# Performance work log

Measured on AMD Instinct MI355X. Metric: run time of the kernel, lower is better.

The kernel has to match this reference:

```python
import jax, jax.numpy as jnp
import numpy as np
import math

N, E, C, NB, NEL, NG = 8192, 131072, 64, 8, 4, 16
R_MAX, AVG_NEI, P_CUT, NL, SH = 5.0, 16.0, 6, 2, 16


def _sph(u):
    # real spherical harmonics l=0..3, component normalization (sum_m Y_lm^2 = 2l+1 on unit sphere)
    x, y, z = u[:, 0], u[:, 1], u[:, 2]
    s3, s15, s5 = math.sqrt(3.0), math.sqrt(15.0), math.sqrt(5.0)
    s105, s7 = math.sqrt(105.0), math.sqrt(7.0)
    c35, c21 = math.sqrt(35.0 / 8.0), math.sqrt(21.0 / 8.0)
    Y = [jnp.ones_like(x),
         s3 * x, s3 * y, s3 * z,
         s15 * x * y, s15 * y * z, 0.5 * s5 * (3 * z * z - 1), s15 * x * z, 0.5 * s15 * (x * x - y * y),
         c35 * y * (3 * x * x - y * y), s105 * x * y * z, c21 * y * (5 * z * z - 1),
         0.5 * s7 * (5 * z ** 3 - 3 * z), c21 * x * (5 * z * z - 1),
         0.5 * s105 * z * (x * x - y * y), c35 * x * (x * x - 3 * y * y)]
    return jnp.stack(Y, axis=-1)  # [E,16]


def _bessel(r):
    k = jnp.arange(1, NB + 1, dtype=r.dtype)
    return math.sqrt(2.0 / R_MAX) * jnp.sin(k * jnp.pi * r[:, None] / R_MAX) / r[:, None]


def _poly_cutoff(r):
    p = float(P_CUT)
    x = r / R_MAX
    f = (1.0 - 0.5 * (p + 1) * (p + 2) * x ** p + p * (p + 2) * x ** (p + 1)
         - 0.5 * p * (p + 1) * x ** (p + 2))
    return f * (x < 1.0)


def setup_inputs() -> dict:
    key = jax.random.key(0)
    ks = jax.random.split(key, 16)
    sc = lambda fan: 1.0 / math.sqrt(fan)
    return {
        "pos": 2.0 * jax.random.normal(ks[0], (N, 3), jnp.float32),
        "atom_types": jax.random.randint(ks[1], (N,), 0, NEL),
        "edge_index": jax.random.randint(ks[2], (2, E), 0, N),
        "batch": jnp.sort(jax.random.randint(ks[3], (N,), 0, NG)),
        "W_embed": jax.random.normal(ks[4], (NEL, C), jnp.float32),
        "W_r1": sc(NB) * jax.random.normal(ks[5], (NL, NB, 64), jnp.float32),
        "W_r2": sc(64) * jax.random.normal(ks[6], (NL, 64, 64), jnp.float32),
        "W_r3": sc(64) * jax.random.normal(ks[7], (NL, 64, C), jnp.float32),
        "W_sc": sc(C) * jax.random.normal(ks[8], (NL, NEL, C, C), jnp.float32),
        "w_prod": 0.5 * jax.random.normal(ks[9], (NL, NEL, 4), jnp.float32),
        "w_ro0": sc(C) * jax.random.normal(ks[10], (C,), jnp.float32),
        "W_ro1a": sc(C) * jax.random.normal(ks[11], (C, 16), jnp.float32),
        "w_ro1b": sc(16) * jax.random.normal(ks[12], (16,), jnp.float32),
    }


def reference(pos, atom_types, edge_index, batch, W_embed, W_r1, W_r2, W_r3,
              W_sc, w_prod, w_ro0, W_ro1a, w_ro1b):
    src, dst = edge_index[0], edge_index[1]
    vec = pos[dst] - pos[src]                      # [E,3]
    r = jnp.sqrt(jnp.sum(vec * vec, -1) + 1e-12)   # [E]
    Y = _sph(vec / r[:, None])                     # [E,SH]
    edge_feats = _bessel(r) * _poly_cutoff(r)[:, None]  # [E,NB]
    h = W_embed[atom_types]                        # one-hot @ W == lookup, [N,C]
    energies = [jnp.zeros((NG,), pos.dtype)]       # pair_repulsion disabled
    for i in range(NL):
        Rw = jax.nn.silu(edge_feats @ W_r1[i])
        Rw = jax.nn.silu(Rw @ W_r2[i])
        Rw = Rw @ W_r3[i]                          # radial MLP weights [E,C]
        # gather-TP-scatter: message [E,C,SH] -> node A [N,C,SH]
        m = (Rw * h[src])[:, :, None] * Y[:, None, :]
        A = jax.ops.segment_sum(m.reshape(E, C * SH), dst,
                                num_segments=N).reshape(N, C, SH) / AVG_NEI
        sc_feat = jnp.einsum('nc,ncd->nd', h, W_sc[i][atom_types])  # element-dep skip
        inv = jnp.stack([A[:, :, 0],
                         jnp.sum(A[:, :, 1:4] ** 2, -1),
                         jnp.sum(A[:, :, 4:9] ** 2, -1),
                         jnp.sum(A[:, :, 9:16] ** 2, -1)], axis=-1)  # [N,C,4]
        h = jnp.einsum('ncj,nj->nc', inv, w_prod[i][atom_types]) + sc_feat
        if i < NL - 1:
            e_node = h @ w_ro0                     # linear readout
        else:
            e_node = jax.nn.silu(h @ W_ro1a) @ w_ro1b  # gated MLP readout
        energies.append(jax.ops.segment_sum(e_node, batch, num_segments=NG))
    contributions = jnp.stack(energies, -1)        # [NG, NL+1]
    return jnp.sum(contributions, -1)              # total energy per graph
```

## Files before the change

kernel.cpp:

```cpp
#include <hip/hip_runtime.h>
#include <hip/hip_bf16.h>
#include <math.h>

#define N_NODES 8192
#define N_EDGES 131072
#define NGRP 16
#define NLAY 2
#define NELM 4
#define SLOT_STRIDE 64
#define N_SLOTS (N_NODES*SLOT_STRIDE)
constexpr float INV_AVG = 1.0f / 16.0f;
constexpr float PI_F = 3.14159265358979323846f;

#define CV_EMB   0
#define CV_SC    256
#define CV_PROD  33024
#define CV_RO0   33056
#define CV_RO1A  33120
#define CV_RO1B  34144
#define CV_SC0T  34160
#define CVT_WORK 34160
#define CVT_N    34416

#define SWZ_PER_L 10240
#define SWZ_N     20480

#define B_GEOM 512
#define B_CVT  134
#define B_SWZ  80
#define SETUP_GRID (B_GEOM + B_CVT + B_SWZ + 1)

typedef __hip_bfloat16 bf16;
typedef __attribute__((ext_vector_type(8))) short bf16x8;
typedef __attribute__((ext_vector_type(4))) float f32x4;

__device__ __forceinline__ float silu_f(float x){ return x / (1.0f + __expf(-x)); }
__device__ __forceinline__ float bfbits2f(unsigned short u){
  return __uint_as_float(((unsigned)u) << 16);
}
__device__ __forceinline__ void unpack2(unsigned u, float& lo, float& hi){
  lo = __uint_as_float(u << 16);
  hi = __uint_as_float(u & 0xffff0000u);
}
__device__ __forceinline__ short f2bs(float v){
  union { bf16 b; short s; } u; u.b = __float2bfloat16(v); return u.s;
}
__device__ __forceinline__ float ldf(const void* p, int i, int flag){
  if (flag) return bfbits2f(((const unsigned short*)p)[i]);
  return ((const float*)p)[i];
}
__device__ __forceinline__ int detect_fl(const void* pos){
  int lane = threadIdx.x & 63;
  const unsigned short* u = (const unsigned short*)pos;
  float va = bfbits2f(u[2*lane]), vb = bfbits2f(u[2*lane+1]);
  bool bad = !(fabsf(va) <= 1000.0f) || !(fabsf(vb) <= 1000.0f);
  return (__ballot(bad) == 0ull) ? 1 : 0;
}
__device__ __forceinline__ void WSYNC(){ __builtin_amdgcn_wave_barrier(); }

__device__ __forceinline__ void gl_lds4(const void* g, void* l){
  __builtin_amdgcn_global_load_lds(
      (const __attribute__((address_space(1))) unsigned*)g,
      (__attribute__((address_space(3))) unsigned*)l, 4, 0, 0);
}

__global__ void k_setup(const void* __restrict__ pos, const int* __restrict__ types,
                        const int* __restrict__ ei,
                        const void* __restrict__ Wemb, const void* __restrict__ Wsc,
                        const void* __restrict__ wprod, const void* __restrict__ wro0,
                        const void* __restrict__ Wro1a, const void* __restrict__ wro1b,
                        const void* __restrict__ Wr1, const void* __restrict__ Wr2,
                        const void* __restrict__ Wr3,
                        int* __restrict__ cursor, uint4* __restrict__ meta,
                        unsigned short* __restrict__ Yb,
                        float* __restrict__ cv, short* __restrict__ swz){
  int b = blockIdx.x, tix = threadIdx.x;
  int fl = detect_fl(pos);
  if (b < B_GEOM){
    int e = b*256 + tix;
    int s = ei[e], d = ei[N_EDGES + e];
    int slot = (d << 6) + atomicAdd(&cursor[d], 1);
    float vx = ldf(pos, d*3+0, fl) - ldf(pos, s*3+0, fl);
    float vy = ldf(pos, d*3+1, fl) - ldf(pos, s*3+1, fl);
    float vz = ldf(pos, d*3+2, fl) - ldf(pos, s*3+2, fl);
    float r = sqrtf(vx*vx + vy*vy + vz*vz + 1e-12f);
    float ir = 1.0f / r;
    float x = vx*ir, y = vy*ir, z = vz*ir;
    const float s3 = 1.7320508075688772f, s15 = 3.872983346207417f, s5 = 2.23606797749979f;
    const float s105 = 10.246950765959598f, s7 = 2.6457513110645907f;
    const float c35 = 2.091650066335189f, c21 = 1.6201851746019651f;
    float x2 = x*x, y2 = y*y, z2 = z*z;
    float ys[16] = {
      1.0f, s3*x, s3*y, s3*z,
      s15*x*y, s15*y*z, 0.5f*s5*(3.0f*z2-1.0f), s15*x*z,
      0.5f*s15*(x2-y2), c35*y*(3.0f*x2-y2), s105*x*y*z, c21*y*(5.0f*z2-1.0f),
      0.5f*s7*(5.0f*z2*z-3.0f*z), c21*x*(5.0f*z2-1.0f), 0.5f*s105*z*(x2-y2),
      c35*x*(x2-3.0f*y2) };
    union { bf16 bb[16]; uint4 u[2]; } pk;
#pragma unroll
    for (int k = 0; k < 16; k++) pk.bb[k] = __float2bfloat16(ys[k]);
    uint4* yp = (uint4*)(Yb + (size_t)e*16);
    yp[0] = pk.u[0];
    yp[1] = pk.u[1];
    meta[slot] = make_uint4((unsigned)s | ((unsigned)types[s] << 16),
                            (unsigned)e, __float_as_uint(r), 0u);
    return;
  }
  if (b < B_GEOM + B_CVT){
    int i = (b - B_GEOM)*256 + tix;
    if (i < 256)  { cv[CV_EMB + i] = ldf(Wemb, i, fl); return; }
    if (i < 33024){ int j=i-256;   cv[CV_SC  + j] = ldf(Wsc,  j, fl); return; }
    if (i < 33056){ int j=i-33024; cv[CV_PROD+ j] = ldf(wprod,j, fl); return; }
    if (i < 33120){ int j=i-33056; cv[CV_RO0 + j] = ldf(wro0, j, fl); return; }
    if (i < 34144){ int j=i-33120; cv[CV_RO1A+ j] = ldf(Wro1a,j, fl); return; }
    if (i < CVT_WORK){ int j=i-34144; cv[CV_RO1B+ j] = ldf(wro1b,j, fl); return; }
    return;
  }
  if (b < B_GEOM + B_CVT + B_SWZ){
    int i = (b - B_GEOM - B_CVT)*256 + tix;
    int l = i / SWZ_PER_L, w = i % SWZ_PER_L;
    float v;
    if (w < 2048){
      int t = w >> 9, q = (w >> 7) & 3, n = (w >> 3) & 15, j = w & 7;
      int k = q*8 + j;
      v = (k < 8) ? ldf(Wr1, l*512 + k*64 + t*16 + n, fl) : 0.0f;
    } else if (w < 6144){
      int w2 = w - 2048;
      int nt = w2 >> 10, kt = (w2 >> 9) & 1, q = (w2 >> 7) & 3, n = (w2 >> 3) & 15, j = w2 & 7;
      int k = kt*32 + q*8 + j;
      v = ldf(Wr2, l*4096 + k*64 + nt*16 + n, fl);
    } else {
      int w3 = w - 6144;
      int nt = w3 >> 10, kt = (w3 >> 9) & 1, q = (w3 >> 7) & 3, n = (w3 >> 3) & 15, j = w3 & 7;
      int k = kt*32 + q*8 + j;
      v = ldf(Wr3, l*4096 + k*64 + nt*16 + n, fl);
    }
    swz[i] = f2bs(v);
    return;
  }
  {
    int ty = tix >> 6, d = tix & 63;
    float s = 0.0f;
#pragma unroll 8
    for (int c = 0; c < 64; c++)
      s += ldf(Wemb, ty*64 + c, fl) * ldf(Wsc, ty*4096 + c*64 + d, fl);
    cv[CV_SC0T + tix] = s;
  }
}

#define ROWS 72
template<int LAYER_KIND>
__global__ void __launch_bounds__(64) k_gu(const short* __restrict__ sw,
        const uint4* __restrict__ meta,
        const float* __restrict__ h_old,
        float* __restrict__ h_new, const unsigned short* __restrict__ Yb,
        const int* __restrict__ cursor, const int* __restrict__ types,
        const float* __restrict__ Wsc, const float* __restrict__ wprod,
        const float* __restrict__ wemb, const float* __restrict__ sc0t,
        const float* __restrict__ wro0,
        const float* __restrict__ Wro1a, const float* __restrict__ wro1b,
        const int* __restrict__ batch, float* __restrict__ ene2){
  __shared__ __align__(16) short A_[16*ROWS];
  __shared__ __align__(16) float hS[LAYER_KIND ? 16 : 1][64];
  __shared__ __align__(16) unsigned short yS[16][16];
  __shared__ float hn_l[64];
  int lane = threadIdx.x;
  int q = lane >> 4, nn = lane & 15;
  int n = blockIdx.x;
  int beg = n << 6;
  short* A = A_;

  const bf16x8* S1 = (const bf16x8*)(sw);
  const bf16x8* S2 = (const bf16x8*)(sw + 2048);
  const bf16x8* S3 = (const bf16x8*)(sw + 6144);

  float e0=0.f, e1=0.f, e2=0.f, e3=0.f;
  if (LAYER_KIND == 0){
    e0 = wemb[lane]; e1 = wemb[64+lane]; e2 = wemb[128+lane]; e3 = wemb[192+lane];
  }

  int dcnt = cursor[n];
  uint4 mC = meta[beg + nn];
  int end = beg + dcnt;

  float acc[16];
#pragma unroll
  for (int s = 0; s < 16; s++) acc[s] = 0.0f;

  int cb = beg;
  do {
    int cnt = min(16, end - cb);
    WSYNC();
    int ev = (int)mC.y;
    {
      int er0 = __shfl(ev, (lane >> 3)) & (N_EDGES - 1);
      gl_lds4((const char*)Yb + (size_t)er0*32 + (lane & 7)*4, &yS[0][0]);
      int er1 = __shfl(ev, 8 + (lane >> 3)) & (N_EDGES - 1);
      gl_lds4((const char*)Yb + (size_t)er1*32 + (lane & 7)*4, &yS[8][0]);
    }
    int tv = (int)((mC.x >> 16) & 3u);
    if (LAYER_KIND == 1){
      int sv = (int)(mC.x & 0xFFFFu);
      for (int i = 0; i < cnt; i++){
        int src = __builtin_amdgcn_readlane(sv, i) & (N_NODES - 1);
        gl_lds4(h_old + (size_t)src*64 + lane, &hS[i][0]);
      }
    }
    float rv = __uint_as_float(mC.z);
    uint4 mN = meta[min(cb + 16 + nn, N_SLOTS - 1)];
    {
      float r = rv;
      float xc = r * 0.2f;
      float f = 0.0f;
      if (xc < 1.0f){
        float x3 = xc*xc*xc, x6 = x3*x3, x7 = x6*xc, x8 = x7*xc;
        f = 1.0f - 28.0f*x6 + 48.0f*x7 - 21.0f*x8;
      }
      float bs = 0.6324555320336759f * f / r;
      float t0 = PI_F * r * 0.2f;
      bf16x8 af1 = {0,0,0,0,0,0,0,0};
      if (q == 0){
#pragma unroll
        for (int j = 0; j < 8; j++) af1[j] = f2bs(bs * __sinf((float)(j+1) * t0));
      }
      f32x4 macc[4];
#pragma unroll
      for (int t = 0; t < 4; t++){
        bf16x8 b = S1[t*64 + q*16 + nn];
        f32x4 z = {0.f,0.f,0.f,0.f};
        macc[t] = __builtin_amdgcn_mfma_f32_16x16x32_bf16(af1, b, z, 0, 0, 0);
      }
#pragma unroll
      for (int t = 0; t < 4; t++)
#pragma unroll
        for (int rg = 0; rg < 4; rg++)
          A[(q*4+rg)*ROWS + t*16 + nn] = f2bs(silu_f(macc[t][rg]));
      WSYNC();
      bf16x8 a0 = *(const bf16x8*)&A[nn*ROWS + 0*32 + q*8];
      bf16x8 a1 = *(const bf16x8*)&A[nn*ROWS + 1*32 + q*8];
      WSYNC();
#pragma unroll
      for (int t = 0; t < 4; t++){
        f32x4 z = {0.f,0.f,0.f,0.f};
        bf16x8 b0 = S2[t*128 + 0*64 + q*16 + nn];
        bf16x8 b1 = S2[t*128 + 1*64 + q*16 + nn];
        z = __builtin_amdgcn_mfma_f32_16x16x32_bf16(a0, b0, z, 0, 0, 0);
        z = __builtin_amdgcn_mfma_f32_16x16x32_bf16(a1, b1, z, 0, 0, 0);
        macc[t] = z;
      }
#pragma unroll
      for (int t = 0; t < 4; t++)
#pragma unroll
        for (int rg = 0; rg < 4; rg++)
          A[(q*4+rg)*ROWS + t*16 + nn] = f2bs(silu_f(macc[t][rg]));
      WSYNC();
      a0 = *(const bf16x8*)&A[nn*ROWS + 0*32 + q*8];
      a1 = *(const bf16x8*)&A[nn*ROWS + 1*32 + q*8];
      WSYNC();
#pragma unroll
      for (int t = 0; t < 4; t++){
        f32x4 z = {0.f,0.f,0.f,0.f};
        bf16x8 b0 = S3[t*128 + 0*64 + q*16 + nn];
        bf16x8 b1 = S3[t*128 + 1*64 + q*16 + nn];
        z = __builtin_amdgcn_mfma_f32_16x16x32_bf16(a0, b0, z, 0, 0, 0);
        z = __builtin_amdgcn_mfma_f32_16x16x32_bf16(a1, b1, z, 0, 0, 0);
        macc[t] = z;
      }
#pragma unroll
      for (int t = 0; t < 4; t++)
#pragma unroll
        for (int rg = 0; rg < 4; rg++)
          A[(q*4+rg)*ROWS + t*16 + nn] = f2bs(macc[t][rg]);
      WSYNC();
    }
    asm volatile("s_waitcnt vmcnt(0)" ::: "memory");
    __builtin_amdgcn_sched_barrier(0);
    for (int i = 0; i < cnt; i++){
      float rw = bfbits2f((unsigned short)A[i*ROWS + lane]);
      float hv;
      if (LAYER_KIND == 0){
        int ty = __builtin_amdgcn_readlane(tv, i);
        hv = (ty & 2) ? ((ty & 1) ? e3 : e2) : ((ty & 1) ? e1 : e0);
      } else {
        hv = hS[i][lane];
      }
      float g = rw * hv;
      const uint4* yq = (const uint4*)&yS[i][0];
      uint4 ya = yq[0], yb = yq[1];
      float lo, hi;
      unpack2(ya.x, lo, hi); acc[0]  += g*lo; acc[1]  += g*hi;
      unpack2(ya.y, lo, hi); acc[2]  += g*lo; acc[3]  += g*hi;
      unpack2(ya.z, lo, hi); acc[4]  += g*lo; acc[5]  += g*hi;
      unpack2(ya.w, lo, hi); acc[6]  += g*lo; acc[7]  += g*hi;
      unpack2(yb.x, lo, hi); acc[8]  += g*lo; acc[9]  += g*hi;
      unpack2(yb.y, lo, hi); acc[10] += g*lo; acc[11] += g*hi;
      unpack2(yb.z, lo, hi); acc[12] += g*lo; acc[13] += g*hi;
      unpack2(yb.w, lo, hi); acc[14] += g*lo; acc[15] += g*hi;
    }
    mC = mN;
    cb += 16;
  } while (cb < end);
#pragma unroll
  for (int s = 0; s < 16; s++) acc[s] *= INV_AVG;

  int ty = __builtin_amdgcn_readfirstlane(types[n]);
  float sc;
  if (LAYER_KIND == 0){
    sc = sc0t[ty*64 + lane];
  } else {
    const float* Ws = Wsc + (size_t)ty*4096;
    const float* hrow = h_old + (size_t)n*64;
    float sc0 = 0.f, sc1 = 0.f, sc2 = 0.f, sc3 = 0.f;
#pragma unroll
    for (int c = 0; c < 64; c += 4){
      sc0 += hrow[c+0] * Ws[(c+0)*64 + lane];
      sc1 += hrow[c+1] * Ws[(c+1)*64 + lane];
      sc2 += hrow[c+2] * Ws[(c+2)*64 + lane];
      sc3 += hrow[c+3] * Ws[(c+3)*64 + lane];
    }
    sc = (sc0 + sc1) + (sc2 + sc3);
  }

  float inv0 = acc[0];
  float inv1 = acc[1]*acc[1] + acc[2]*acc[2] + acc[3]*acc[3];
  float inv2 = acc[4]*acc[4] + acc[5]*acc[5] + acc[6]*acc[6] + acc[7]*acc[7]
             + acc[8]*acc[8];
  float inv3 = acc[9]*acc[9] + acc[10]*acc[10] + acc[11]*acc[11] + acc[12]*acc[12]
             + acc[13]*acc[13] + acc[14]*acc[14] + acc[15]*acc[15];
  const float* wp = wprod + ty*4;
  float hn = inv0*wp[0] + inv1*wp[1] + inv2*wp[2] + inv3*wp[3] + sc;
  if (LAYER_KIND == 0)
    h_new[(size_t)n*64 + lane] = hn;

  float ev_;
  if (LAYER_KIND == 0){
    float p = hn * wro0[lane];
#pragma unroll
    for (int off = 32; off >= 1; off >>= 1) p += __shfl_xor(p, off, 64);
    ev_ = p;
  } else {
    hn_l[lane] = hn;
    WSYNC();
    int j = lane & 15;
    float pj = 0.0f;
#pragma unroll
    for (int c = 0; c < 64; c++)
      pj += hn_l[c] * Wro1a[c*16 + j];
    float evj = silu_f(pj) * wro1b[j];
    evj += __shfl_xor(evj, 8, 64);
    evj += __shfl_xor(evj, 4, 64);
    evj += __shfl_xor(evj, 2, 64);
    evj += __shfl_xor(evj, 1, 64);
    ev_ = evj;
  }
  if (lane == 0) atomicAdd(&ene2[(n & 7)*NGRP + batch[n]], ev_);
}

__global__ void k_out(const float* __restrict__ ene2, const void* __restrict__ pos,
                      void* __restrict__ out){
  int fl = detect_fl(pos);
  int t = threadIdx.x;
  if (t < NGRP){
    float v = 0.0f;
#pragma unroll
    for (int k = 0; k < 8; k++) v += ene2[k*NGRP + t];
    if (fl) ((bf16*)out)[t] = __float2bfloat16(v);
    else    ((float*)out)[t] = v;
  }
}

static inline size_t rup(size_t x){ return (x + 255) & ~(size_t)255; }

extern "C" void kernel_launch(void* const* d_in, const int* in_sizes, int n_in,
                              void* d_out, int out_size, void* d_ws, size_t ws_size,
                              hipStream_t stream) {
  const void* pos   = d_in[0];
  const int*  types = (const int*)d_in[1];
  const int*  ei    = (const int*)d_in[2];
  const int*  batch = (const int*)d_in[3];
  const void* Wemb  = d_in[4];
  const void* Wr1   = d_in[5];
  const void* Wr2   = d_in[6];
  const void* Wr3   = d_in[7];
  const void* Wsc   = d_in[8];
  const void* wprod = d_in[9];
  const void* wro0  = d_in[10];
  const void* Wro1a = d_in[11];
  const void* wro1b = d_in[12];

  char* w = (char*)d_ws;
  float* ene2     = (float*)w; w += 512;
  int*   cursor   = (int*)  w; w += rup((size_t)N_NODES*4);
  float* cv       = (float*)w; w += rup((size_t)CVT_N*4);
  short* swz      = (short*)w; w += rup((size_t)SWZ_N*2);
  uint4* meta     = (uint4*)w; w += rup((size_t)N_SLOTS*16) + 256;
  float* hbuf     = (float*)w; w += rup((size_t)N_NODES*64*4);
  unsigned short* Yb = (unsigned short*)w; w += rup((size_t)N_EDGES*16*2);
  w += 4096;

  hipMemsetAsync(ene2, 0, 512 + (size_t)N_NODES*4, stream);

  k_setup<<<SETUP_GRID, 256, 0, stream>>>(pos, types, ei,
      Wemb, Wsc, wprod, wro0, Wro1a, wro1b, Wr1, Wr2, Wr3,
      cursor, meta, Yb, cv, swz);

  k_gu<0><<<N_NODES, 64, 0, stream>>>(swz, meta,
      hbuf , hbuf , Yb, cursor, types,
      cv + CV_SC, cv + CV_PROD, cv + CV_EMB, cv + CV_SC0T,
      cv + CV_RO0, cv + CV_RO1A, cv + CV_RO1B, batch, ene2);
  k_gu<1><<<N_NODES, 64, 0, stream>>>(swz + SWZ_PER_L, meta,
      hbuf , hbuf , Yb, cursor, types,
      cv + CV_SC + (size_t)NELM*4096, cv + CV_PROD + NELM*4, cv + CV_EMB,
      cv + CV_SC0T, cv + CV_RO0, cv + CV_RO1A, cv + CV_RO1B, batch, ene2);

  k_out<<<1, 64, 0, stream>>>(ene2, pos, d_out);
}
```

Measured before the change: 165.9 us.

## Double-buffer edge gathers and hoist skip-connection ahead of message loop

Issues the spherical-harmonic and neighbour-feature gathers for the next edge chunk into a second LDS buffer while the current chunk is processed. The metadata prefetch moves two chunks ahead. The element-dependent skip matmul moves before the edge loop so its loads overlap the first gathers. The readout dot product is split across the four lane groups and reduced with shuffles instead of a 64-long serial loop per lane. This doubles the LDS staging buffers, which may affect occupancy, and adds more in-flight loads and registers.

Result: slower. 200.8 us (+21.0%).

```diff
diff --git a/kernel.cpp b/kernel.cpp
--- a/kernel.cpp
+++ b/kernel.cpp
@@ -161,8 +161,9 @@
         const float* __restrict__ Wro1a, const float* __restrict__ wro1b,
         const int* __restrict__ batch, float* __restrict__ ene2){
   __shared__ __align__(16) short A_[16*ROWS];
-  __shared__ __align__(16) float hS[LAYER_KIND ? 16 : 1][64];
-  __shared__ __align__(16) unsigned short yS[16][16];
+  __shared__ __align__(16) float hS[LAYER_KIND ? 2 : 1]
+                                   [LAYER_KIND ? 16 : 1][64];
+  __shared__ __align__(16) unsigned short yS[2][16][16];
   __shared__ float hn_l[64];
   int lane = threadIdx.x;
   int q = lane >> 4, nn = lane & 15;
@@ -181,35 +182,54 @@
 
   int dcnt = cursor[n];
   uint4 mC = meta[beg + nn];
+  uint4 mN = meta[min(beg + 16 + nn, N_SLOTS - 1)];
   int end = beg + dcnt;
 
+  {
+    int evp = (int)mC.y;
+    int er0 = __shfl(evp, (lane >> 3)) & (N_EDGES - 1);
+    gl_lds4((const char*)Yb + (size_t)er0*32 + (lane & 7)*4, &yS[0][0][0]);
+    int er1 = __shfl(evp, 8 + (lane >> 3)) & (N_EDGES - 1);
+    gl_lds4((const char*)Yb + (size_t)er1*32 + (lane & 7)*4, &yS[0][8][0]);
+    if (LAYER_KIND == 1){
+      int svp = (int)(mC.x & 0xFFFFu);
+      int cnt0 = min(16, dcnt);
+      for (int i = 0; i < cnt0; i++){
+        int src = __builtin_amdgcn_readlane(svp, i) & (N_NODES - 1);
+        gl_lds4(h_old + (size_t)src*64 + lane, &hS[0][i][0]);
+      }
+    }
+  }
+
+  int ty = __builtin_amdgcn_readfirstlane(types[n]);
+  float sc;
+  if (LAYER_KIND == 0){
+    sc = sc0t[ty*64 + lane];
+  } else {
+    const float* Ws = Wsc + (size_t)ty*4096;
+    const float* hrow = h_old + (size_t)n*64;
+    float sc0 = 0.f, sc1 = 0.f, sc2 = 0.f, sc3 = 0.f;
+#pragma unroll
+    for (int c = 0; c < 64; c += 4){
+      sc0 += hrow[c+0] * Ws[(c+0)*64 + lane];
+      sc1 += hrow[c+1] * Ws[(c+1)*64 + lane];
+      sc2 += hrow[c+2] * Ws[(c+2)*64 + lane];
+      sc3 += hrow[c+3] * Ws[(c+3)*64 + lane];
+    }
+    sc = (sc0 + sc1) + (sc2 + sc3);
+  }
+
   float acc[16];
 #pragma unroll
   for (int s = 0; s < 16; s++) acc[s] = 0.0f;
 
   int cb = beg;
+  int bufsel = 0;
   do {
     int cnt = min(16, end - cb);
     WSYNC();
-    int ev = (int)mC.y;
     {
-      int er0 = __shfl(ev, (lane >> 3)) & (N_EDGES - 1);
-      gl_lds4((const char*)Yb + (size_t)er0*32 + (lane & 7)*4, &yS[0][0]);
-      int er1 = __shfl(ev, 8 + (lane >> 3)) & (N_EDGES - 1);
-      gl_lds4((const char*)Yb + (size_t)er1*32 + (lane & 7)*4, &yS[8][0]);
-    }
-    int tv = (int)((mC.x >> 16) & 3u);
-    if (LAYER_KIND == 1){
-      int sv = (int)(mC.x & 0xFFFFu);
-      for (int i = 0; i < cnt; i++){
-        int src = __builtin_amdgcn_readlane(sv, i) & (N_NODES - 1);
-        gl_lds4(h_old + (size_t)src*64 + lane, &hS[i][0]);
-      }
-    }
-    float rv = __uint_as_float(mC.z);
-    uint4 mN = meta[min(cb + 16 + nn, N_SLOTS - 1)];
-    {
-      float r = rv;
+      float r = __uint_as_float(mC.z);
       float xc = r * 0.2f;
       float f = 0.0f;
       if (xc < 1.0f){
@@ -275,17 +295,37 @@
     }
     asm volatile("s_waitcnt vmcnt(0)" ::: "memory");
     __builtin_amdgcn_sched_barrier(0);
+    int more = (cb + 16) < end;
+    if (more){
+      int evp = (int)mN.y;
+      int er0 = __shfl(evp, (lane >> 3)) & (N_EDGES - 1);
+      gl_lds4((const char*)Yb + (size_t)er0*32 + (lane & 7)*4,
+              &yS[bufsel ^ 1][0][0]);
+      int er1 = __shfl(evp, 8 + (lane >> 3)) & (N_EDGES - 1);
+      gl_lds4((const char*)Yb + (size_t)er1*32 + (lane & 7)*4,
+              &yS[bufsel ^ 1][8][0]);
+      if (LAYER_KIND == 1){
+        int svp = (int)(mN.x & 0xFFFFu);
+        int cntn = min(16, end - (cb + 16));
+        for (int i = 0; i < cntn; i++){
+          int src = __builtin_amdgcn_readlane(svp, i) & (N_NODES - 1);
+          gl_lds4(h_old + (size_t)src*64 + lane, &hS[bufsel ^ 1][i][0]);
+        }
+      }
+    }
+    uint4 m2 = meta[min(cb + 32 + nn, N_SLOTS - 1)];
+    int tv = (int)((mC.x >> 16) & 3u);
     for (int i = 0; i < cnt; i++){
       float rw = bfbits2f((unsigned short)A[i*ROWS + lane]);
       float hv;
       if (LAYER_KIND == 0){
-        int ty = __builtin_amdgcn_readlane(tv, i);
-        hv = (ty & 2) ? ((ty & 1) ? e3 : e2) : ((ty & 1) ? e1 : e0);
+        int tyi = __builtin_amdgcn_readlane(tv, i);
+        hv = (tyi & 2) ? ((tyi & 1) ? e3 : e2) : ((tyi & 1) ? e1 : e0);
       } else {
-        hv = hS[i][lane];
+        hv = hS[bufsel][i][lane];
       }
       float g = rw * hv;
-      const uint4* yq = (const uint4*)&yS[i][0];
+      const uint4* yq = (const uint4*)&yS[bufsel][i][0];
       uint4 ya = yq[0], yb = yq[1];
       float lo, hi;
       unpack2(ya.x, lo, hi); acc[0]  += g*lo; acc[1]  += g*hi;
@@ -297,29 +337,11 @@
       unpack2(yb.z, lo, hi); acc[12] += g*lo; acc[13] += g*hi;
       unpack2(yb.w, lo, hi); acc[14] += g*lo; acc[15] += g*hi;
     }
-    mC = mN;
+    mC = mN; mN = m2; bufsel ^= 1;
     cb += 16;
   } while (cb < end);
 #pragma unroll
   for (int s = 0; s < 16; s++) acc[s] *= INV_AVG;
-
-  int ty = __builtin_amdgcn_readfirstlane(types[n]);
-  float sc;
-  if (LAYER_KIND == 0){
-    sc = sc0t[ty*64 + lane];
-  } else {
-    const float* Ws = Wsc + (size_t)ty*4096;
-    const float* hrow = h_old + (size_t)n*64;
-    float sc0 = 0.f, sc1 = 0.f, sc2 = 0.f, sc3 = 0.f;
-#pragma unroll
-    for (int c = 0; c < 64; c += 4){
-      sc0 += hrow[c+0] * Ws[(c+0)*64 + lane];
-      sc1 += hrow[c+1] * Ws[(c+1)*64 + lane];
-      sc2 += hrow[c+2] * Ws[(c+2)*64 + lane];
-      sc3 += hrow[c+3] * Ws[(c+3)*64 + lane];
-    }
-    sc = (sc0 + sc1) + (sc2 + sc3);
-  }
 
   float inv0 = acc[0];
   float inv1 = acc[1]*acc[1] + acc[2]*acc[2] + acc[3]*acc[3];
@@ -341,11 +363,15 @@
   } else {
     hn_l[lane] = hn;
     WSYNC();
-    int j = lane & 15;
+    int j = lane & 15, qq = lane >> 4;
     float pj = 0.0f;
 #pragma unroll
-    for (int c = 0; c < 64; c++)
+    for (int c0 = 0; c0 < 16; c0++){
+      int c = qq*16 + c0;
       pj += hn_l[c] * Wro1a[c*16 + j];
+    }
+    pj += __shfl_xor(pj, 16, 64);
+    pj += __shfl_xor(pj, 32, 64);
     float evj = silu_f(pj) * wro1b[j];
     evj += __shfl_xor(evj, 8, 64);
     evj += __shfl_xor(evj, 4, 64);
```
